# Performance work log

Measured on AMD Instinct MI355X. Metric: run time of the kernel, lower is better.

The kernel has to match this reference:

```python
import jax, jax.numpy as jnp
import numpy as np

N_NODES = 100000
N_EDGES = 1000000
HIDDEN = 64
IN_DIM = 4


def setup_inputs() -> dict:
    key = jax.random.key(0)
    ks = jax.random.split(key, 7)
    x = jax.random.normal(ks[0], (N_NODES, IN_DIM), dtype=jnp.float32)
    edges = jax.random.randint(ks[1], (N_EDGES, 2), 0, N_NODES, dtype=jnp.int32)
    W1 = jax.random.normal(ks[2], (IN_DIM, HIDDEN), dtype=jnp.float32) * 0.5
    b1 = jax.random.normal(ks[3], (HIDDEN,), dtype=jnp.float32) * 0.1
    phases = jax.random.normal(ks[4], (N_EDGES,), dtype=jnp.float32) * 0.1
    Wout = jax.random.normal(ks[5], (HIDDEN, 1), dtype=jnp.float32) * 0.1
    bout = jax.random.normal(ks[6], (1,), dtype=jnp.float32) * 0.1
    return {"x": x, "edges": edges, "W1": W1, "b1": b1,
            "phases": phases, "Wout": Wout, "bout": bout}


def reference(x, edges, W1, b1, phases, Wout, bout):
    # h = lin(x): [N, D]
    h = x @ W1 + b1
    u = edges[:, 0]  # [E]
    v = edges[:, 1]  # [E]
    c = jnp.cos(phases)  # [E]
    s = jnp.sin(phases)  # [E]
    hu = h[u]  # [E, D] gather
    hv = h[v]  # [E, D] gather
    # rot only mixes the first two channels; the rest pass through (eye).
    # msg to v: rot @ h[u] -> [c*h0 - s*h1, s*h0 + c*h1, h2, ...]
    msg_v = jnp.concatenate([
        (c * hu[:, 0] - s * hu[:, 1])[:, None],
        (s * hu[:, 0] + c * hu[:, 1])[:, None],
        hu[:, 2:],
    ], axis=1)
    # msg to u: rot.T @ h[v] -> [c*h0 + s*h1, -s*h0 + c*h1, h2, ...]
    msg_u = jnp.concatenate([
        (c * hv[:, 0] + s * hv[:, 1])[:, None],
        (-s * hv[:, 0] + c * hv[:, 1])[:, None],
        hv[:, 2:],
    ], axis=1)
    diffused = jnp.zeros_like(h).at[v].add(msg_v).at[u].add(msg_u)  # scatter-add
    return (h + diffused) @ Wout + bout  # [N, 1]
```

## Files before the change

### kernel.cpp

```cpp
#include <hip/hip_runtime.h>

#define N_NODES 100000
#define N_EDGES 1000000
#define HIDDEN 64

#define S_SHARDS 256
#define C_SHARD 391
#define EPB 2048
#define NBLK ((N_EDGES + EPB - 1) / EPB)
#define CAP 48
#define A_THREADS 512
#define B_THREADS 512

__device__ __forceinline__ void compute_consts(
    const float* __restrict__ W1, const float* __restrict__ b1,
    const float* __restrict__ Wout, const float* __restrict__ bout,
    float* kc, int tid) {
    if (tid < 64) {
        float wj = Wout[tid];
        float p0 = W1[0 * HIDDEN + tid] * wj;
        float p1 = W1[1 * HIDDEN + tid] * wj;
        float p2 = W1[2 * HIDDEN + tid] * wj;
        float p3 = W1[3 * HIDDEN + tid] * wj;
        float pb = b1[tid] * wj;
        #pragma unroll
        for (int off = 32; off > 0; off >>= 1) {
            p0 += __shfl_down(p0, off);
            p1 += __shfl_down(p1, off);
            p2 += __shfl_down(p2, off);
            p3 += __shfl_down(p3, off);
            pb += __shfl_down(pb, off);
        }
        if (tid < 4) {
            kc[5 + tid] = W1[tid * HIDDEN + 0];
            kc[9 + tid] = W1[tid * HIDDEN + 1];
        }
        if (tid == 0) {
            kc[0] = p0; kc[1] = p1; kc[2] = p2; kc[3] = p3; kc[4] = pb;
            kc[13] = b1[0]; kc[14] = b1[1];
            kc[15] = Wout[0]; kc[16] = Wout[1];
            kc[17] = bout[0];
        }
    }
}

__global__ __launch_bounds__(A_THREADS) void binA_kernel(
    const int2* __restrict__ edges, const float* __restrict__ phases,
    const float4* __restrict__ x4,
    const float* __restrict__ W1, const float* __restrict__ b1,
    const float* __restrict__ Wout, const float* __restrict__ bout,
    int* __restrict__ countsT,
    int2* __restrict__ records) {
    __shared__ int cnt[S_SHARDS];
    __shared__ float kc[18];
    const int tid = threadIdx.x;

    compute_consts(W1, b1, Wout, bout, kc, tid);
    if (tid < S_SHARDS) cnt[tid] = 0;
    __syncthreads();

    const float c0 = kc[0], c1 = kc[1], c2 = kc[2], c3 = kc[3], cb = kc[4];
    const float a0 = kc[5], a1 = kc[6], a2 = kc[7], a3 = kc[8];
    const float g0 = kc[9], g1 = kc[10], g2 = kc[11], g3 = kc[12];
    const float b10 = kc[13], b11 = kc[14], w0 = kc[15], w1 = kc[16];

    const int e0 = blockIdx.x * EPB;
    const int e1 = min(e0 + EPB, N_EDGES);
    int2* __restrict__ myrec = records + (size_t)blockIdx.x * S_SHARDS * CAP;

    for (int e = e0 + tid; e < e1; e += A_THREADS) {
        int2 ed = edges[e];
        float ph = phases[e];
        float sn, cs;
        __sincosf(ph, &sn, &cs);
        float4 xu = x4[ed.x];
        float4 xv = x4[ed.y];

        float h0u = xu.x * a0 + xu.y * a1 + xu.z * a2 + xu.w * a3 + b10;
        float h1u = xu.x * g0 + xu.y * g1 + xu.z * g2 + xu.w * g3 + b11;
        float du  = xu.x * c0 + xu.y * c1 + xu.z * c2 + xu.w * c3 + cb;
        float au = h0u * w0 + h1u * w1;
        float bu = h0u * w1 - h1u * w0;
        float to_v = cs * au + sn * bu + (du - au);

        float h0v = xv.x * a0 + xv.y * a1 + xv.z * a2 + xv.w * a3 + b10;
        float h1v = xv.x * g0 + xv.y * g1 + xv.z * g2 + xv.w * g3 + b11;
        float dv  = xv.x * c0 + xv.y * c1 + xv.z * c2 + xv.w * c3 + cb;
        float av = h0v * w0 + h1v * w1;
        float bv = h0v * w1 - h1v * w0;
        float to_u = cs * av - sn * bv + (dv - av);

        int sv = ed.y / C_SHARD;
        int su = ed.x / C_SHARD;
        int pv = atomicAdd(&cnt[sv], 1);
        int pu = atomicAdd(&cnt[su], 1);
        if (pv < CAP) myrec[sv * CAP + pv] = make_int2(ed.y, __float_as_int(to_v));
        if (pu < CAP) myrec[su * CAP + pu] = make_int2(ed.x, __float_as_int(to_u));
    }
    __syncthreads();
    if (tid < S_SHARDS) countsT[tid * NBLK + blockIdx.x] = min(cnt[tid], CAP);
}

__global__ __launch_bounds__(B_THREADS) void binB_kernel(
    const float4* __restrict__ x4,
    const float* __restrict__ W1, const float* __restrict__ b1,
    const float* __restrict__ Wout, const float* __restrict__ bout,
    const int* __restrict__ countsT, const int2* __restrict__ records,
    float* __restrict__ out) {
    __shared__ float bins[C_SHARD];
    __shared__ float kc[18];
    const int tid = threadIdx.x;
    const int s = blockIdx.x;

    compute_consts(W1, b1, Wout, bout, kc, tid);
    for (int j = tid; j < C_SHARD; j += B_THREADS) bins[j] = 0.0f;
    __syncthreads();

    const int nbase = s * C_SHARD;
    for (int b = tid; b < NBLK; b += B_THREADS) {
        int c = countsT[s * NBLK + b];
        const int2* __restrict__ rec = records + ((size_t)b * S_SHARDS + s) * CAP;
        for (int j = 0; j < c; j++) {
            int2 it = rec[j];
            atomicAdd(&bins[it.x - nbase], __int_as_float(it.y));
        }
    }
    __syncthreads();

    const float c0 = kc[0], c1 = kc[1], c2 = kc[2], c3 = kc[3];
    const float cb = kc[4], bo = kc[17];
    for (int j = tid; j < C_SHARD; j += B_THREADS) {
        int n = nbase + j;
        if (n < N_NODES) {
            float4 xi = x4[n];
            out[n] = bins[j] + xi.x * c0 + xi.y * c1 + xi.z * c2 + xi.w * c3 + cb + bo;
        }
    }
}

__global__ void precompute_kernel(const float* __restrict__ W1,
                                  const float* __restrict__ b1,
                                  const float* __restrict__ Wout,
                                  const float* __restrict__ bout,
                                  float* __restrict__ consts) {
    __shared__ float kc[18];
    compute_consts(W1, b1, Wout, bout, kc, threadIdx.x);
    __syncthreads();
    if (threadIdx.x < 18) consts[threadIdx.x] = kc[threadIdx.x];
}

__global__ void edge_atomic_kernel(const int2* __restrict__ edges,
                                   const float* __restrict__ phases,
                                   const float4* __restrict__ x4,
                                   const float* __restrict__ consts,
                                   float* __restrict__ rep) {
    int e = blockIdx.x * blockDim.x + threadIdx.x;
    if (e >= N_EDGES) return;
    float c0 = consts[0], c1 = consts[1], c2 = consts[2], c3 = consts[3];
    float cb = consts[4];
    float a0 = consts[5], a1 = consts[6], a2 = consts[7], a3 = consts[8];
    float g0 = consts[9], g1 = consts[10], g2 = consts[11], g3 = consts[12];
    float b10 = consts[13], b11 = consts[14], w0 = consts[15], w1 = consts[16];
    int2 ed = edges[e];
    float ph = phases[e];
    float sn, cs;
    __sincosf(ph, &sn, &cs);
    float4 xu = x4[ed.x];
    float4 xv = x4[ed.y];
    float h0u = xu.x * a0 + xu.y * a1 + xu.z * a2 + xu.w * a3 + b10;
    float h1u = xu.x * g0 + xu.y * g1 + xu.z * g2 + xu.w * g3 + b11;
    float du  = xu.x * c0 + xu.y * c1 + xu.z * c2 + xu.w * c3 + cb;
    float au = h0u * w0 + h1u * w1;
    float bu = h0u * w1 - h1u * w0;
    float h0v = xv.x * a0 + xv.y * a1 + xv.z * a2 + xv.w * a3 + b10;
    float h1v = xv.x * g0 + xv.y * g1 + xv.z * g2 + xv.w * g3 + b11;
    float dv  = xv.x * c0 + xv.y * c1 + xv.z * c2 + xv.w * c3 + cb;
    float av = h0v * w0 + h1v * w1;
    float bv = h0v * w1 - h1v * w0;
    atomicAdd(rep + ed.y, cs * au + sn * bu + (du - au));
    atomicAdd(rep + ed.x, cs * av - sn * bv + (dv - av));
}

__global__ void reduce_kernel(const float4* __restrict__ x4,
                              const float* __restrict__ consts,
                              const float* __restrict__ rep,
                              float* __restrict__ out) {
    int i = blockIdx.x * blockDim.x + threadIdx.x;
    if (i >= N_NODES) return;
    float c0 = consts[0], c1 = consts[1], c2 = consts[2], c3 = consts[3];
    float cb = consts[4], bo = consts[17];
    float4 xi = x4[i];
    out[i] = rep[i] + xi.x * c0 + xi.y * c1 + xi.z * c2 + xi.w * c3 + cb + bo;
}

extern "C" void kernel_launch(void* const* d_in, const int* in_sizes, int n_in,
                              void* d_out, int out_size, void* d_ws, size_t ws_size,
                              hipStream_t stream) {
    const float* x      = (const float*)d_in[0];
    const int*   edges  = (const int*)d_in[1];
    const float* W1     = (const float*)d_in[2];
    const float* b1     = (const float*)d_in[3];
    const float* phases = (const float*)d_in[4];
    const float* Wout   = (const float*)d_in[5];
    const float* bout   = (const float*)d_in[6];
    float* out = (float*)d_out;

    const size_t counts_bytes = (size_t)S_SHARDS * NBLK * sizeof(int);
    const size_t rec_off      = 1u << 19;
    const size_t rec_bytes    = (size_t)NBLK * S_SHARDS * CAP * sizeof(int2);
    (void)counts_bytes;

    if (ws_size >= rec_off + rec_bytes) {
        int*  countsT = (int*)d_ws;
        int2* records = (int2*)((char*)d_ws + rec_off);
        binA_kernel<<<NBLK, A_THREADS, 0, stream>>>(
            (const int2*)edges, phases, (const float4*)x,
            W1, b1, Wout, bout, countsT, records);
        binB_kernel<<<S_SHARDS, B_THREADS, 0, stream>>>(
            (const float4*)x, W1, b1, Wout, bout, countsT, records, out);
    } else {
        float* consts = (float*)d_ws;
        float* rep    = (float*)((char*)d_ws + 256);
        hipMemsetAsync(rep, 0, N_NODES * sizeof(float), stream);
        precompute_kernel<<<1, 64, 0, stream>>>(W1, b1, Wout, bout, consts);
        edge_atomic_kernel<<<(N_EDGES + 255) / 256, 256, 0, stream>>>(
            (const int2*)edges, phases, (const float4*)x, consts, rep);
        reduce_kernel<<<(N_NODES + 255) / 256, 256, 0, stream>>>(
            (const float4*)x, consts, rep, out);
    }
}
```

Before: 114.7 us.

## Replace two-pass record binning with per-range shared-memory histograms and slice reduction

The edge-to-shard record binning (per-block record buffers with a fixed capacity, then a per-shard accumulation pass) is replaced. Now 7 node ranges × 64 edge slices of blocks each scan their edge slice and accumulate contributions into a 57KB shared-memory bin array for that range, then write dense partials. A second kernel sums the 64 slice partials per node and adds the self term. This removes the scattered record writes and capped-overflow handling. In exchange, every edge is read 7 times, and about 26MB of dense partials is written and read back. The large shared-memory footprint also limits how many blocks fit per CU.

```diff
diff --git a/kernel.cpp b/kernel.cpp
--- a/kernel.cpp
+++ b/kernel.cpp
@@ -4,13 +4,11 @@
 #define N_EDGES 1000000
 #define HIDDEN 64
 
-#define S_SHARDS 256
-#define C_SHARD 391
-#define EPB 2048
-#define NBLK ((N_EDGES + EPB - 1) / EPB)
-#define CAP 48
+#define N_RANGES 7
+#define C_RANGE 14336
+#define N_SLICES 64
+#define ES ((N_EDGES + N_SLICES - 1) / N_SLICES)
 #define A_THREADS 512
-#define B_THREADS 512
 
 __device__ __forceinline__ void compute_consts(
     const float* __restrict__ W1, const float* __restrict__ b1,
@@ -44,19 +42,20 @@
     }
 }
 
-__global__ __launch_bounds__(A_THREADS) void binA_kernel(
+__global__ __launch_bounds__(A_THREADS) void range_kernel(
     const int2* __restrict__ edges, const float* __restrict__ phases,
     const float4* __restrict__ x4,
     const float* __restrict__ W1, const float* __restrict__ b1,
     const float* __restrict__ Wout, const float* __restrict__ bout,
-    int* __restrict__ countsT,
-    int2* __restrict__ records) {
-    __shared__ int cnt[S_SHARDS];
+    float* __restrict__ part) {
+    __shared__ float bins[C_RANGE];
     __shared__ float kc[18];
     const int tid = threadIdx.x;
+    const int r = blockIdx.x / N_SLICES;
+    const int s = blockIdx.x % N_SLICES;
 
     compute_consts(W1, b1, Wout, bout, kc, tid);
-    if (tid < S_SHARDS) cnt[tid] = 0;
+    for (int j = tid; j < C_RANGE; j += A_THREADS) bins[j] = 0.0f;
     __syncthreads();
 
     const float c0 = kc[0], c1 = kc[1], c2 = kc[2], c3 = kc[3], cb = kc[4];
@@ -64,78 +63,63 @@
     const float g0 = kc[9], g1 = kc[10], g2 = kc[11], g3 = kc[12];
     const float b10 = kc[13], b11 = kc[14], w0 = kc[15], w1 = kc[16];
 
-    const int e0 = blockIdx.x * EPB;
-    const int e1 = min(e0 + EPB, N_EDGES);
-    int2* __restrict__ myrec = records + (size_t)blockIdx.x * S_SHARDS * CAP;
+    const int nlo = r * C_RANGE;
+    const int e0 = s * ES;
+    const int e1 = min(e0 + ES, N_EDGES);
 
     for (int e = e0 + tid; e < e1; e += A_THREADS) {
         int2 ed = edges[e];
-        float ph = phases[e];
-        float sn, cs;
-        __sincosf(ph, &sn, &cs);
-        float4 xu = x4[ed.x];
-        float4 xv = x4[ed.y];
-
-        float h0u = xu.x * a0 + xu.y * a1 + xu.z * a2 + xu.w * a3 + b10;
-        float h1u = xu.x * g0 + xu.y * g1 + xu.z * g2 + xu.w * g3 + b11;
-        float du  = xu.x * c0 + xu.y * c1 + xu.z * c2 + xu.w * c3 + cb;
-        float au = h0u * w0 + h1u * w1;
-        float bu = h0u * w1 - h1u * w0;
-        float to_v = cs * au + sn * bu + (du - au);
-
-        float h0v = xv.x * a0 + xv.y * a1 + xv.z * a2 + xv.w * a3 + b10;
-        float h1v = xv.x * g0 + xv.y * g1 + xv.z * g2 + xv.w * g3 + b11;
-        float dv  = xv.x * c0 + xv.y * c1 + xv.z * c2 + xv.w * c3 + cb;
-        float av = h0v * w0 + h1v * w1;
-        float bv = h0v * w1 - h1v * w0;
-        float to_u = cs * av - sn * bv + (dv - av);
-
-        int sv = ed.y / C_SHARD;
-        int su = ed.x / C_SHARD;
-        int pv = atomicAdd(&cnt[sv], 1);
-        int pu = atomicAdd(&cnt[su], 1);
-        if (pv < CAP) myrec[sv * CAP + pv] = make_int2(ed.y, __float_as_int(to_v));
-        if (pu < CAP) myrec[su * CAP + pu] = make_int2(ed.x, __float_as_int(to_u));
+        unsigned ju = (unsigned)(ed.x - nlo);
+        unsigned jv = (unsigned)(ed.y - nlo);
+        if (ju < C_RANGE || jv < C_RANGE) {
+            float ph = phases[e];
+            float sn, cs;
+            __sincosf(ph, &sn, &cs);
+            if (jv < C_RANGE) {
+                float4 xu = x4[ed.x];
+                float h0 = xu.x * a0 + xu.y * a1 + xu.z * a2 + xu.w * a3 + b10;
+                float h1 = xu.x * g0 + xu.y * g1 + xu.z * g2 + xu.w * g3 + b11;
+                float d  = xu.x * c0 + xu.y * c1 + xu.z * c2 + xu.w * c3 + cb;
+                float a  = h0 * w0 + h1 * w1;
+                float b  = h0 * w1 - h1 * w0;
+                atomicAdd(&bins[jv], cs * a + sn * b + (d - a));
+            }
+            if (ju < C_RANGE) {
+                float4 xv = x4[ed.y];
+                float h0 = xv.x * a0 + xv.y * a1 + xv.z * a2 + xv.w * a3 + b10;
+                float h1 = xv.x * g0 + xv.y * g1 + xv.z * g2 + xv.w * g3 + b11;
+                float d  = xv.x * c0 + xv.y * c1 + xv.z * c2 + xv.w * c3 + cb;
+                float a  = h0 * w0 + h1 * w1;
+                float b  = h0 * w1 - h1 * w0;
+                atomicAdd(&bins[ju], cs * a - sn * b + (d - a));
+            }
+        }
     }
     __syncthreads();
-    if (tid < S_SHARDS) countsT[tid * NBLK + blockIdx.x] = min(cnt[tid], CAP);
-}
-
-__global__ __launch_bounds__(B_THREADS) void binB_kernel(
+
+    float* __restrict__ dst = part + (size_t)blockIdx.x * C_RANGE;
+    for (int j = tid; j < C_RANGE; j += A_THREADS) dst[j] = bins[j];
+}
+
+__global__ __launch_bounds__(A_THREADS) void reduce_kernel(
     const float4* __restrict__ x4,
     const float* __restrict__ W1, const float* __restrict__ b1,
     const float* __restrict__ Wout, const float* __restrict__ bout,
-    const int* __restrict__ countsT, const int2* __restrict__ records,
-    float* __restrict__ out) {
-    __shared__ float bins[C_SHARD];
+    const float* __restrict__ part, float* __restrict__ out) {
     __shared__ float kc[18];
-    const int tid = threadIdx.x;
-    const int s = blockIdx.x;
-
-    compute_consts(W1, b1, Wout, bout, kc, tid);
-    for (int j = tid; j < C_SHARD; j += B_THREADS) bins[j] = 0.0f;
-    __syncthreads();
-
-    const int nbase = s * C_SHARD;
-    for (int b = tid; b < NBLK; b += B_THREADS) {
-        int c = countsT[s * NBLK + b];
-        const int2* __restrict__ rec = records + ((size_t)b * S_SHARDS + s) * CAP;
-        for (int j = 0; j < c; j++) {
-            int2 it = rec[j];
-            atomicAdd(&bins[it.x - nbase], __int_as_float(it.y));
-        }
-    }
-    __syncthreads();
-
-    const float c0 = kc[0], c1 = kc[1], c2 = kc[2], c3 = kc[3];
-    const float cb = kc[4], bo = kc[17];
-    for (int j = tid; j < C_SHARD; j += B_THREADS) {
-        int n = nbase + j;
-        if (n < N_NODES) {
-            float4 xi = x4[n];
-            out[n] = bins[j] + xi.x * c0 + xi.y * c1 + xi.z * c2 + xi.w * c3 + cb + bo;
-        }
-    }
+    compute_consts(W1, b1, Wout, bout, kc, threadIdx.x);
+    __syncthreads();
+    int i = blockIdx.x * A_THREADS + threadIdx.x;
+    if (i >= N_NODES) return;
+    int r = i / C_RANGE;
+    int j = i - r * C_RANGE;
+    const float* __restrict__ p = part + (size_t)r * N_SLICES * C_RANGE + j;
+    float sum = 0.0f;
+    #pragma unroll 8
+    for (int s = 0; s < N_SLICES; s++) sum += p[(size_t)s * C_RANGE];
+    float4 xi = x4[i];
+    out[i] = sum + xi.x * kc[0] + xi.y * kc[1] + xi.z * kc[2] + xi.w * kc[3]
+           + kc[4] + kc[17];
 }
 
 __global__ void precompute_kernel(const float* __restrict__ W1,
@@ -181,16 +165,15 @@
     atomicAdd(rep + ed.x, cs * av - sn * bv + (dv - av));
 }
 
-__global__ void reduce_kernel(const float4* __restrict__ x4,
-                              const float* __restrict__ consts,
-                              const float* __restrict__ rep,
-                              float* __restrict__ out) {
+__global__ void final_kernel(const float4* __restrict__ x4,
+                             const float* __restrict__ consts,
+                             const float* __restrict__ rep,
+                             float* __restrict__ out) {
     int i = blockIdx.x * blockDim.x + threadIdx.x;
     if (i >= N_NODES) return;
-    float c0 = consts[0], c1 = consts[1], c2 = consts[2], c3 = consts[3];
-    float cb = consts[4], bo = consts[17];
     float4 xi = x4[i];
-    out[i] = rep[i] + xi.x * c0 + xi.y * c1 + xi.z * c2 + xi.w * c3 + cb + bo;
+    out[i] = rep[i] + xi.x * consts[0] + xi.y * consts[1] + xi.z * consts[2]
+           + xi.w * consts[3] + consts[4] + consts[17];
 }
 
 extern "C" void kernel_launch(void* const* d_in, const int* in_sizes, int n_in,
@@ -205,19 +188,15 @@
     const float* bout   = (const float*)d_in[6];
     float* out = (float*)d_out;
 
-    const size_t counts_bytes = (size_t)S_SHARDS * NBLK * sizeof(int);
-    const size_t rec_off      = 1u << 19;
-    const size_t rec_bytes    = (size_t)NBLK * S_SHARDS * CAP * sizeof(int2);
-    (void)counts_bytes;
-
-    if (ws_size >= rec_off + rec_bytes) {
-        int*  countsT = (int*)d_ws;
-        int2* records = (int2*)((char*)d_ws + rec_off);
-        binA_kernel<<<NBLK, A_THREADS, 0, stream>>>(
+    const size_t part_bytes = (size_t)N_RANGES * N_SLICES * C_RANGE * sizeof(float);
+
+    if (ws_size >= part_bytes) {
+        float* part = (float*)d_ws;
+        range_kernel<<<N_RANGES * N_SLICES, A_THREADS, 0, stream>>>(
             (const int2*)edges, phases, (const float4*)x,
-            W1, b1, Wout, bout, countsT, records);
-        binB_kernel<<<S_SHARDS, B_THREADS, 0, stream>>>(
-            (const float4*)x, W1, b1, Wout, bout, countsT, records, out);
+            W1, b1, Wout, bout, part);
+        reduce_kernel<<<(N_NODES + A_THREADS - 1) / A_THREADS, A_THREADS, 0, stream>>>(
+            (const float4*)x, W1, b1, Wout, bout, part, out);
     } else {
         float* consts = (float*)d_ws;
         float* rep    = (float*)((char*)d_ws + 256);
@@ -225,7 +204,7 @@
         precompute_kernel<<<1, 64, 0, stream>>>(W1, b1, Wout, bout, consts);
         edge_atomic_kernel<<<(N_EDGES + 255) / 256, 256, 0, stream>>>(
             (const int2*)edges, phases, (const float4*)x, consts, rep);
-        reduce_kernel<<<(N_NODES + 255) / 256, 256, 0, stream>>>(
+        final_kernel<<<(N_NODES + 255) / 256, 256, 0, stream>>>(
             (const float4*)x, consts, rep, out);
     }
 }
```

After: 118.6 us. +3.4%, slower.
